# Optimization experiments

Measured on AMD Instinct MI355X. Metric: run time of the kernel, lower is better.

## Reference

```python
import jax, jax.numpy as jnp
import numpy as np
from jax.ops import segment_sum, segment_max

N, E, H, C = 20000, 320000, 4, 128
G, NF, EF, GF = 1024, 9, 4, 50
EPS = 1e-5
NEG_SLOPE = 0.2


def setup_inputs() -> dict:
    key = jax.random.key(0)
    ks = jax.random.split(key, 16)
    inp = {
        'x': jax.random.normal(ks[0], (N, NF), jnp.float32),
        'edge_attr': jax.random.normal(ks[1], (E, EF), jnp.float32),
        'global_feat': jax.random.normal(ks[2], (G, GF), jnp.float32),
        'Wl1': jax.random.normal(ks[3], (NF, H * C), jnp.float32) * 0.1,
        'Wr1': jax.random.normal(ks[4], (NF, H * C), jnp.float32) * 0.1,
        'We1': jax.random.normal(ks[5], (EF, H * C), jnp.float32) * 0.1,
        'att1': jax.random.normal(ks[6], (H, C), jnp.float32) * 0.1,
        'b1': jax.random.normal(ks[7], (H * C,), jnp.float32) * 0.01,
        'gamma1': jnp.ones((H * C,), jnp.float32),
        'beta1': jnp.zeros((H * C,), jnp.float32),
        'mean1': jnp.zeros((H * C,), jnp.float32),
        'var1': jnp.ones((H * C,), jnp.float32),
        'Wl2': jax.random.normal(ks[8], (H * C, H * C), jnp.float32) * 0.05,
        'Wr2': jax.random.normal(ks[9], (H * C, H * C), jnp.float32) * 0.05,
        'We2': jax.random.normal(ks[10], (EF, H * C), jnp.float32) * 0.1,
        'att2': jax.random.normal(ks[11], (H, C), jnp.float32) * 0.1,
        'b2': jax.random.normal(ks[12], (H * C,), jnp.float32) * 0.01,
        'gamma2': jnp.ones((H * C,), jnp.float32),
        'beta2': jnp.zeros((H * C,), jnp.float32),
        'mean2': jnp.zeros((H * C,), jnp.float32),
        'var2': jnp.ones((H * C,), jnp.float32),
        'fc1_w': jax.random.normal(ks[13], (H * C + GF, C), jnp.float32) * 0.05,
        'fc1_b': jnp.zeros((C,), jnp.float32),
        'fc2_w': jax.random.normal(ks[14], (C, 1), jnp.float32) * 0.1,
        'fc2_b': jnp.zeros((1,), jnp.float32),
        'edge_index': jax.random.randint(ks[15], (2, E), 0, N, jnp.int32),
        'batch': jnp.sort(jax.random.randint(jax.random.fold_in(key, 99), (N,), 0, G, jnp.int32)),
    }
    return inp


def gatv2_layer(x, src, dst, ea, Wl, Wr, We, att, bias):
    # PyG GATv2Conv: add self-loops with fill_value='mean' edge_attr
    n = x.shape[0]
    loop = jnp.arange(n, dtype=src.dtype)
    deg = segment_sum(jnp.ones((src.shape[0],), x.dtype), dst, num_segments=n)
    ea_mean = segment_sum(ea, dst, num_segments=n) / jnp.clip(deg, 1.0)[:, None]
    s = jnp.concatenate([src, loop])
    d = jnp.concatenate([dst, loop])
    eat = jnp.concatenate([ea, ea_mean], axis=0)
    xl = (x @ Wl).reshape(n, H, C)  # source transform
    xr = (x @ Wr).reshape(n, H, C)  # target transform
    ee = (eat @ We).reshape(-1, H, C)
    e = jax.nn.leaky_relu(xl[s] + xr[d] + ee, NEG_SLOPE)  # [E+N, H, C]
    logits = jnp.einsum('ehc,hc->eh', e, att)  # [E+N, H]
    m = segment_max(logits, d, num_segments=n)  # stable segment softmax
    ex = jnp.exp(logits - m[d])
    alpha = ex / segment_sum(ex, d, num_segments=n)[d]
    out = segment_sum(alpha[..., None] * xl[s], d, num_segments=n)  # [N, H, C]
    return out.reshape(n, H * C) + bias


def batch_norm(x, g, b, mu, var):
    return (x - mu) * jax.lax.rsqrt(var + EPS) * g + b


def reference(x, edge_attr, global_feat, Wl1, Wr1, We1, att1, b1, gamma1, beta1, mean1, var1,
              Wl2, Wr2, We2, att2, b2, gamma2, beta2, mean2, var2,
              fc1_w, fc1_b, fc2_w, fc2_b, edge_index, batch):
    src, dst = edge_index[0], edge_index[1]
    h = jax.nn.relu(batch_norm(gatv2_layer(x, src, dst, edge_attr, Wl1, Wr1, We1, att1, b1),
                               gamma1, beta1, mean1, var1))
    h = jax.nn.relu(batch_norm(gatv2_layer(h, src, dst, edge_attr, Wl2, Wr2, We2, att2, b2),
                               gamma2, beta2, mean2, var2))
    cnt = segment_sum(jnp.ones((h.shape[0],), h.dtype), batch, num_segments=G)
    pooled = segment_sum(h, batch, num_segments=G) / jnp.clip(cnt, 1.0)[:, None]  # [G, H*C]
    z = jnp.concatenate([pooled, global_feat], axis=1)
    z = jax.nn.relu(z @ fc1_w + fc1_b)
    return (z @ fc2_w + fc2_b).squeeze()
```

## Files before the change

### kernel.cpp

```cpp
#include <hip/hip_runtime.h>
#include <hip/hip_bf16.h>

#define Nn 20000
#define Ee 320000
#define Hh 4
#define Cc 128
#define HC 512
#define Gg 1024
#define NFt 9
#define EFt 4
#define GFt 50
#define EPSf 1e-5f
#define SLOPE 0.2f

typedef __attribute__((ext_vector_type(8))) short bf16x8;
typedef __attribute__((ext_vector_type(4))) float f32x4;
typedef __attribute__((ext_vector_type(2))) float f32x2;
typedef __attribute__((ext_vector_type(4))) unsigned ui32x4;

typedef const __attribute__((address_space(1))) unsigned char* gp1_t;
typedef __attribute__((address_space(3))) unsigned char* lp3_t;
__device__ __forceinline__ void gload16(const void* g, void* l) {
    __builtin_amdgcn_global_load_lds((gp1_t)g, (lp3_t)l, 16, 0, 0);
}

__device__ __forceinline__ float bf2f(short s) {
    return __uint_as_float(((unsigned)(unsigned short)s) << 16);
}

__device__ __forceinline__ f32x2 pkfma(f32x2 a, f32x2 b, f32x2 c) {
    f32x2 d;
    asm("v_pk_fma_f32 %0, %1, %2, %3" : "=v"(d) : "v"(a), "v"(b), "v"(c));
    return d;
}
__device__ __forceinline__ f32x2 pkadd(f32x2 a, f32x2 b) {
    f32x2 d;
    asm("v_pk_add_f32 %0, %1, %2" : "=v"(d) : "v"(a), "v"(b));
    return d;
}
__device__ __forceinline__ f32x2 pkmul(f32x2 a, f32x2 b) {
    f32x2 d;
    asm("v_pk_mul_f32 %0, %1, %2" : "=v"(d) : "v"(a), "v"(b));
    return d;
}
__device__ __forceinline__ int bperm(int byteaddr, int v) {
    return __builtin_amdgcn_ds_bpermute(byteaddr, v);
}
__device__ __forceinline__ float bpermf(int byteaddr, float v) {
    return __int_as_float(__builtin_amdgcn_ds_bpermute(byteaddr, __float_as_int(v)));
}

__global__ __launch_bounds__(256) void k_setup(
    const int* __restrict__ dst, int* __restrict__ deg, int* __restrict__ rank,
    const int* __restrict__ batch, int* __restrict__ gofs,
    const float* __restrict__ Wl2, const float* __restrict__ Wr2,
    __hip_bfloat16* __restrict__ Wt,
    const float* __restrict__ x, const float* __restrict__ Wl1,
    const float* __restrict__ Wr1, __hip_bfloat16* __restrict__ xl,
    __hip_bfloat16* __restrict__ xr) {
    __shared__ float tile[64][65];
    int b = blockIdx.x, t = threadIdx.x;
    if (b < 1250) {
        int e = b * 256 + t;
        if (e < Ee) rank[e] = atomicAdd(&deg[dst[e]], 1);
    } else if (b < 1329) {
        int i = (b - 1250) * 256 + t;
        if (i >= Nn) return;
        int bb = batch[i];
        if (i == 0) {
            for (int g = 0; g <= bb; ++g) gofs[g] = 0;
        } else {
            int bp = batch[i - 1];
            for (int g = bp + 1; g <= bb; ++g) gofs[g] = i;
        }
        if (i == Nn - 1) {
            for (int g = bb + 1; g <= Gg; ++g) gofs[g] = Nn;
        }
    } else if (b < 1457) {
        int tid = b - 1329;
        int tc = (tid >> 3) * 64;
        int tk = (tid & 7) * 64;
        int lc = t & 63, lr = t >> 6;
        const float* W = (tc < 512) ? Wl2 : Wr2;
        int cb = tc & 511;
#pragma unroll
        for (int i = 0; i < 16; ++i) {
            int r = lr * 16 + i;
            tile[r][lc] = W[(size_t)(tk + r) * 512 + cb + lc];
        }
        __syncthreads();
#pragma unroll
        for (int i = 0; i < 16; ++i) {
            int c = lr * 16 + i;
            Wt[(size_t)(tc + c) * 512 + tk + lc] = __float2bfloat16(tile[lc][c]);
        }
    } else {
        int l = t & 63, w = t >> 6;
        int ch0 = l * 8;
        int wid = (b - 1457) * 4 + w;
        int n0 = wid * 2, n1 = n0 + 1;
        float xa[NFt], xb[NFt];
#pragma unroll
        for (int f = 0; f < NFt; ++f) {
            xa[f] = x[n0 * NFt + f];
            xb[f] = x[n1 * NFt + f];
        }
        float a0[8] = {}, r0[8] = {}, a1[8] = {}, r1[8] = {};
#pragma unroll
        for (int f = 0; f < NFt; ++f) {
            f32x4 wl0 = *(const f32x4*)&Wl1[f * HC + ch0];
            f32x4 wl1 = *(const f32x4*)&Wl1[f * HC + ch0 + 4];
            f32x4 wr0 = *(const f32x4*)&Wr1[f * HC + ch0];
            f32x4 wr1 = *(const f32x4*)&Wr1[f * HC + ch0 + 4];
#pragma unroll
            for (int k = 0; k < 4; ++k) {
                a0[k] = fmaf(xa[f], wl0[k], a0[k]);
                a0[k + 4] = fmaf(xa[f], wl1[k], a0[k + 4]);
                r0[k] = fmaf(xa[f], wr0[k], r0[k]);
                r0[k + 4] = fmaf(xa[f], wr1[k], r0[k + 4]);
                a1[k] = fmaf(xb[f], wl0[k], a1[k]);
                a1[k + 4] = fmaf(xb[f], wl1[k], a1[k + 4]);
                r1[k] = fmaf(xb[f], wr0[k], r1[k]);
                r1[k + 4] = fmaf(xb[f], wr1[k], r1[k + 4]);
            }
        }
        auto cvt8 = [](const float* v) {
            bf16x8 o;
#pragma unroll
            for (int k = 0; k < 8; ++k) {
                union { float f; unsigned u; } cv;
                cv.f = v[k];
                unsigned r = (cv.u + 0x7fff + ((cv.u >> 16) & 1)) >> 16;
                o[k] = (short)r;
            }
            return o;
        };
        *(bf16x8*)(xl + (size_t)n0 * HC + ch0) = cvt8(a0);
        *(bf16x8*)(xr + (size_t)n0 * HC + ch0) = cvt8(r0);
        *(bf16x8*)(xl + (size_t)n1 * HC + ch0) = cvt8(a1);
        *(bf16x8*)(xr + (size_t)n1 * HC + ch0) = cvt8(r1);
    }
}

__global__ void k_scan(const int* __restrict__ deg, int* __restrict__ rowptr) {
    __shared__ int sums[1024];
    int t = threadIdx.x;
    const int n = Nn;
    int chunk = (n + 1023) / 1024;
    int start = t * chunk;
    int lim = min(start + chunk, n);
    int s = 0;
    for (int i = start; i < lim; ++i) s += deg[i];
    sums[t] = s;
    __syncthreads();
    for (int off = 1; off < 1024; off <<= 1) {
        int v = (t >= off) ? sums[t - off] : 0;
        __syncthreads();
        sums[t] += v;
        __syncthreads();
    }
    int run = (t == 0) ? 0 : sums[t - 1];
    for (int i = start; i < lim; ++i) { rowptr[i] = run; run += deg[i]; }
    if (t == 1023) rowptr[n] = sums[1023];
}

__global__ void k_scatter(const int* __restrict__ src, const int* __restrict__ dst,
                          const float* __restrict__ ea, const int* __restrict__ rowptr,
                          const int* __restrict__ rank, int* __restrict__ csr_src,
                          float4* __restrict__ ea_s) {
    int e = blockIdx.x * 256 + threadIdx.x;
    if (e >= Ee) return;
    int pos = rowptr[dst[e]] + rank[e];
    csr_src[pos] = src[e];
    ea_s[pos] = ((const float4*)ea)[e];
}

__global__ __launch_bounds__(256) void k_gemm_mfma(const short* __restrict__ Abf,
                                                   const short* __restrict__ Bt,
                                                   __hip_bfloat16* __restrict__ xl,
                                                   __hip_bfloat16* __restrict__ xr, int M) {
    __shared__ short As[128 * 32];
    __shared__ short Bs[128 * 32];
    int tid = threadIdx.x;
    int l = tid & 63;
    int wid = tid >> 6;
    int bm0 = blockIdx.x * 128;
    int bn0 = blockIdx.y * 128;
    int wr = (wid >> 1) * 64;
    int wc = (wid & 1) * 64;
    f32x4 acc[4][4] = {};

    int srow = l >> 2;
    int skoff = ((l & 3) ^ ((l >> 3) & 3)) * 8;
    int rk = (((l >> 4) ^ (l >> 1)) & 3) * 8;

    for (int k0 = 0; k0 < 512; k0 += 32) {
        {
            int c = wid;
            long row = min(bm0 + c * 16 + srow, M - 1);
            gload16(Abf + row * 512 + k0 + skoff, &As[c * 512]);
            int col = bn0 + c * 16 + srow;
            gload16(Bt + (size_t)col * 512 + k0 + skoff, &Bs[c * 512]);
            c = wid + 4;
            row = min(bm0 + c * 16 + srow, M - 1);
            gload16(Abf + row * 512 + k0 + skoff, &As[c * 512]);
            col = bn0 + c * 16 + srow;
            gload16(Bt + (size_t)col * 512 + k0 + skoff, &Bs[c * 512]);
        }
        asm volatile("s_waitcnt vmcnt(0)" ::: "memory");
        __syncthreads();
        bf16x8 af[4], bfr[4];
#pragma unroll
        for (int m = 0; m < 4; ++m)
            af[m] = *(const bf16x8*)&As[(wr + m * 16 + (l & 15)) * 32 + rk];
#pragma unroll
        for (int n = 0; n < 4; ++n)
            bfr[n] = *(const bf16x8*)&Bs[(wc + n * 16 + (l & 15)) * 32 + rk];
#pragma unroll
        for (int m = 0; m < 4; ++m)
#pragma unroll
            for (int n = 0; n < 4; ++n)
                acc[m][n] = __builtin_amdgcn_mfma_f32_16x16x32_bf16(af[m], bfr[n],
                                                                    acc[m][n], 0, 0, 0);
        __syncthreads();
    }
    __hip_bfloat16* dst = (bn0 < 512) ? xl : xr;
    int cb = bn0 & 511;
#pragma unroll
    for (int m = 0; m < 4; ++m) {
#pragma unroll
        for (int n = 0; n < 4; ++n) {
            int col = cb + wc + n * 16 + (l & 15);
#pragma unroll
            for (int r = 0; r < 4; ++r) {
                int row = bm0 + wr + m * 16 + (l >> 4) * 4 + r;
                if (row < M) dst[(size_t)row * 512 + col] = __float2bfloat16(acc[m][n][r]);
            }
        }
    }
}

__global__ __launch_bounds__(256) void k_fused_attn(
    const __hip_bfloat16* __restrict__ xl, const __hip_bfloat16* __restrict__ xr,
    const float* __restrict__ We, const float* __restrict__ att,
    const int* __restrict__ rowptr, const int* __restrict__ csr_src,
    const float4* __restrict__ ea_s, const float* __restrict__ bias,
    const float* __restrict__ gamma, const float* __restrict__ beta,
    const float* __restrict__ mean, const float* __restrict__ var,
    __hip_bfloat16* __restrict__ hout) {
    int n = blockIdx.x * 4 + (threadIdx.x >> 6);
    if (n >= Nn) return;
    int l = threadIdx.x & 63;
    int ch0 = l * 8;
    const unsigned char* xlb = (const unsigned char*)xl;
    int choff = ch0 * 2;

    f32x2 wee2[4][4], ar2[4], rr2[4];
#pragma unroll
    for (int f = 0; f < 4; ++f) {
        f32x4 w0 = *(const f32x4*)&We[f * HC + ch0];
        f32x4 w1 = *(const f32x4*)&We[f * HC + ch0 + 4];
        wee2[f][0] = (f32x2){w0.x, w0.y};
        wee2[f][1] = (f32x2){w0.z, w0.w};
        wee2[f][2] = (f32x2){w1.x, w1.y};
        wee2[f][3] = (f32x2){w1.z, w1.w};
    }
    {
        f32x4 a0 = *(const f32x4*)&att[ch0];
        f32x4 a1 = *(const f32x4*)&att[ch0 + 4];
        ar2[0] = (f32x2){a0.x, a0.y};
        ar2[1] = (f32x2){a0.z, a0.w};
        ar2[2] = (f32x2){a1.x, a1.y};
        ar2[3] = (f32x2){a1.z, a1.w};
    }
    {
        ui32x4 ru = *(const ui32x4*)(xr + (size_t)n * HC + ch0);
#pragma unroll
        for (int j = 0; j < 4; ++j) {
            unsigned u = ru[j];
            rr2[j] = (f32x2){__uint_as_float(u << 16), __uint_as_float(u & 0xffff0000u)};
        }
    }

    int start = __builtin_amdgcn_readfirstlane(rowptr[n]);
    int nedge = __builtin_amdgcn_readfirstlane(rowptr[n + 1]) - start;

    float m = -1e30f, den = 0.f;
    f32x2 acc2[4] = {};
    float esl0 = 0.f, esl1 = 0.f, esl2 = 0.f, esl3 = 0.f;

    struct Chunk {
        float e[4][4];
        bf16x8 x[4];
    };

    for (int mb = 0; mb < nedge; mb += 64) {
        int cnt = min(64, nedge - mb);
        int msrc = 0;
        float4 mea = make_float4(0.f, 0.f, 0.f, 0.f);
        if (l < cnt) {
            msrc = csr_src[start + mb + l];
            mea = ea_s[start + mb + l];
        }
        esl0 += mea.x; esl1 += mea.y; esl2 += mea.z; esl3 += mea.w;

        auto fetch = [&](Chunk& C, int fb) {
#pragma unroll
            for (int j = 0; j < 4; ++j) {
                int ba = min(fb + j, cnt - 1) * 4;
                int sj = bperm(ba, msrc);
                C.e[j][0] = bpermf(ba, mea.x);
                C.e[j][1] = bpermf(ba, mea.y);
                C.e[j][2] = bpermf(ba, mea.z);
                C.e[j][3] = bpermf(ba, mea.w);
                unsigned voff = ((unsigned)sj << 10) + choff;
                C.x[j] = *(const bf16x8*)(xlb + voff);
            }
        };

        auto compute = [&](const Chunk& C, int base) {
            float p[4];
#pragma unroll
            for (int i = 0; i < 4; ++i) {
                ui32x4 xu = *(const ui32x4*)&C.x[i];
                f32x2 e0p = (f32x2){C.e[i][0], C.e[i][0]};
                f32x2 e1p = (f32x2){C.e[i][1], C.e[i][1]};
                f32x2 e2p = (f32x2){C.e[i][2], C.e[i][2]};
                f32x2 e3p = (f32x2){C.e[i][3], C.e[i][3]};
                f32x2 plin = (f32x2){0.f, 0.f}, pabs = (f32x2){0.f, 0.f};
#pragma unroll
                for (int j = 0; j < 4; ++j) {
                    unsigned u = xu[j];
                    f32x2 xv = (f32x2){__uint_as_float(u << 16),
                                       __uint_as_float(u & 0xffff0000u)};
                    f32x2 z = pkadd(xv, rr2[j]);
                    z = pkfma(e0p, wee2[0][j], z);
                    z = pkfma(e1p, wee2[1][j], z);
                    z = pkfma(e2p, wee2[2][j], z);
                    z = pkfma(e3p, wee2[3][j], z);
                    f32x2 za = (f32x2){fabsf(z.x), fabsf(z.y)};
                    plin = pkfma(ar2[j], z, plin);
                    pabs = pkfma(ar2[j], za, pabs);
                }
                p[i] = 0.6f * (plin.x + plin.y) + 0.4f * (pabs.x + pabs.y);
            }
#pragma unroll
            for (int off = 8; off; off >>= 1) {
                p[0] += __shfl_xor(p[0], off);
                p[1] += __shfl_xor(p[1], off);
                p[2] += __shfl_xor(p[2], off);
                p[3] += __shfl_xor(p[3], off);
            }
#pragma unroll
            for (int i = 1; i < 4; ++i)
                if (base + i >= cnt) p[i] = -1e30f;

            float pmax = fmaxf(fmaxf(p[0], p[1]), fmaxf(p[2], p[3]));
            float ex[4];
            float mloc = m;
            if (!__all(pmax <= mloc + 8.f)) {
                float mn = fmaxf(mloc, pmax);
                float sc = __expf(mloc - mn);
                den *= sc;
                f32x2 scs = (f32x2){sc, sc};
#pragma unroll
                for (int j = 0; j < 4; ++j) acc2[j] = pkmul(acc2[j], scs);
                m = mn;
                mloc = mn;
            }
            ex[0] = __expf(p[0] - mloc); ex[1] = __expf(p[1] - mloc);
            ex[2] = __expf(p[2] - mloc); ex[3] = __expf(p[3] - mloc);
            den += ex[0] + ex[1] + ex[2] + ex[3];
#pragma unroll
            for (int i = 0; i < 4; ++i) {
                f32x2 esp = (f32x2){ex[i], ex[i]};
                ui32x4 xu = *(const ui32x4*)&C.x[i];
#pragma unroll
                for (int j = 0; j < 4; ++j) {
                    unsigned u = xu[j];
                    f32x2 xv = (f32x2){__uint_as_float(u << 16),
                                       __uint_as_float(u & 0xffff0000u)};
                    acc2[j] = pkfma(esp, xv, acc2[j]);
                }
            }
        };

        Chunk A, B;
        fetch(A, 0);
        int base = 0;
        for (;;) {
            fetch(B, base + 4);
            compute(A, base);
            base += 4;
            if (base >= cnt) break;
            fetch(A, base + 4);
            compute(B, base);
            base += 4;
            if (base >= cnt) break;
        }
    }

    {
#pragma unroll
        for (int off = 32; off; off >>= 1) {
            esl0 += __shfl_xor(esl0, off);
            esl1 += __shfl_xor(esl1, off);
            esl2 += __shfl_xor(esl2, off);
            esl3 += __shfl_xor(esl3, off);
        }
        float dv = 1.f / (float)max(nedge, 1);
        f32x2 e0p = (f32x2){esl0 * dv, esl0 * dv};
        f32x2 e1p = (f32x2){esl1 * dv, esl1 * dv};
        f32x2 e2p = (f32x2){esl2 * dv, esl2 * dv};
        f32x2 e3p = (f32x2){esl3 * dv, esl3 * dv};
        ui32x4 xu = *(const ui32x4*)(xl + (size_t)n * HC + ch0);
        f32x2 plin = (f32x2){0.f, 0.f}, pabs = (f32x2){0.f, 0.f};
        f32x2 xv2[4];
#pragma unroll
        for (int j = 0; j < 4; ++j) {
            unsigned u = xu[j];
            xv2[j] = (f32x2){__uint_as_float(u << 16), __uint_as_float(u & 0xffff0000u)};
            f32x2 z = pkadd(xv2[j], rr2[j]);
            z = pkfma(e0p, wee2[0][j], z);
            z = pkfma(e1p, wee2[1][j], z);
            z = pkfma(e2p, wee2[2][j], z);
            z = pkfma(e3p, wee2[3][j], z);
            f32x2 za = (f32x2){fabsf(z.x), fabsf(z.y)};
            plin = pkfma(ar2[j], z, plin);
            pabs = pkfma(ar2[j], za, pabs);
        }
        float pi = 0.6f * (plin.x + plin.y) + 0.4f * (pabs.x + pabs.y);
#pragma unroll
        for (int off = 8; off; off >>= 1) pi += __shfl_xor(pi, off);
        float mn = fmaxf(m, pi);
        float sc = __expf(m - mn);
        float ex = __expf(pi - mn);
        den = den * sc + ex;
        f32x2 scs = (f32x2){sc, sc};
        f32x2 exs = (f32x2){ex, ex};
#pragma unroll
        for (int j = 0; j < 4; ++j) acc2[j] = pkfma(exs, xv2[j], pkmul(acc2[j], scs));
    }

    float iden = 1.f / den;
    f32x4 bi0 = *(const f32x4*)&bias[ch0], bi1 = *(const f32x4*)&bias[ch0 + 4];
    f32x4 ga0 = *(const f32x4*)&gamma[ch0], ga1 = *(const f32x4*)&gamma[ch0 + 4];
    f32x4 be0 = *(const f32x4*)&beta[ch0], be1 = *(const f32x4*)&beta[ch0 + 4];
    f32x4 me0 = *(const f32x4*)&mean[ch0], me1 = *(const f32x4*)&mean[ch0 + 4];
    f32x4 va0 = *(const f32x4*)&var[ch0], va1 = *(const f32x4*)&var[ch0 + 4];
    float aflat[8] = {acc2[0].x, acc2[0].y, acc2[1].x, acc2[1].y,
                      acc2[2].x, acc2[2].y, acc2[3].x, acc2[3].y};
    bf16x8 ob;
#pragma unroll
    for (int k = 0; k < 8; ++k) {
        float bik = (k < 4) ? bi0[k] : bi1[k - 4];
        float gak = (k < 4) ? ga0[k] : ga1[k - 4];
        float bek = (k < 4) ? be0[k] : be1[k - 4];
        float mek = (k < 4) ? me0[k] : me1[k - 4];
        float vak = (k < 4) ? va0[k] : va1[k - 4];
        float Sk = gak * rsqrtf(vak + EPSf);
        float Ok = (bik - mek) * Sk + bek;
        float v = fmaxf(fmaf(aflat[k] * iden, Sk, Ok), 0.f);
        union { float f; unsigned u; } cv;
        cv.f = v;
        unsigned r = (cv.u + 0x7fff + ((cv.u >> 16) & 1)) >> 16;
        ob[k] = (short)r;
    }
    *(bf16x8*)(hout + (size_t)n * HC + ch0) = ob;
}

__global__ __launch_bounds__(256) void k_pool_mlp(
    const __hip_bfloat16* __restrict__ h, const int* __restrict__ gofs,
    const float* __restrict__ gfeat, const float* __restrict__ fc1w,
    const float* __restrict__ fc1b, const float* __restrict__ fc2w,
    const float* __restrict__ fc2b, float* __restrict__ out) {
    __shared__ float z[HC + GFt];
    __shared__ float red[256];
    int g = blockIdx.x, t = threadIdx.x;
    int s = gofs[g], e = gofs[g + 1];
    float a0 = 0.f, a1 = 0.f;
    for (int r = s; r < e; ++r) {
        ushort2 v = ((const ushort2*)(h + (size_t)r * HC))[t];
        a0 += bf2f((short)v.x);
        a1 += bf2f((short)v.y);
    }
    float ic = (e > s) ? 1.f / (float)(e - s) : 0.f;
    z[2 * t] = a0 * ic;
    z[2 * t + 1] = a1 * ic;
    if (t < GFt) z[HC + t] = gfeat[g * GFt + t];
    __syncthreads();
    int c = t & 127, half = t >> 7;
    float acc = (half == 0) ? fc1b[c] : 0.f;
    int j0 = half * 281, j1 = j0 + 281;
    for (int j = j0; j < j1; ++j) acc += z[j] * fc1w[j * 128 + c];
    red[t] = acc;
    __syncthreads();
    if (t < 128) {
        float a = red[t] + red[t + 128];
        red[t] = fmaxf(a, 0.f) * fc2w[t];
    }
    __syncthreads();
    for (int off = 64; off; off >>= 1) {
        if (t < off) red[t] += red[t + off];
        __syncthreads();
    }
    if (t == 0) out[g] = red[0] + fc2b[0];
}

extern "C" void kernel_launch(void* const* d_in, const int* in_sizes, int n_in,
                              void* d_out, int out_size, void* d_ws, size_t ws_size,
                              hipStream_t stream) {
    const float* x = (const float*)d_in[0];
    const float* ea = (const float*)d_in[1];
    const float* gfeat = (const float*)d_in[2];
    const float* Wl1 = (const float*)d_in[3];
    const float* Wr1 = (const float*)d_in[4];
    const float* We1 = (const float*)d_in[5];
    const float* att1 = (const float*)d_in[6];
    const float* b1 = (const float*)d_in[7];
    const float* gamma1 = (const float*)d_in[8];
    const float* beta1 = (const float*)d_in[9];
    const float* mean1 = (const float*)d_in[10];
    const float* var1 = (const float*)d_in[11];
    const float* Wl2 = (const float*)d_in[12];
    const float* Wr2 = (const float*)d_in[13];
    const float* We2 = (const float*)d_in[14];
    const float* att2 = (const float*)d_in[15];
    const float* b2 = (const float*)d_in[16];
    const float* gamma2 = (const float*)d_in[17];
    const float* beta2 = (const float*)d_in[18];
    const float* mean2 = (const float*)d_in[19];
    const float* var2 = (const float*)d_in[20];
    const float* fc1w = (const float*)d_in[21];
    const float* fc1b = (const float*)d_in[22];
    const float* fc2w = (const float*)d_in[23];
    const float* fc2b = (const float*)d_in[24];
    const int* eidx = (const int*)d_in[25];
    const int* batch = (const int*)d_in[26];
    float* out = (float*)d_out;

    const int* srcp = eidx;
    const int* dstp = eidx + Ee;

    char* p = (char*)d_ws;
    auto alloc = [&](size_t bytes) -> char* {
        char* r = p;
        p += (bytes + 255) & ~(size_t)255;
        return r;
    };
    __hip_bfloat16* xl = (__hip_bfloat16*)alloc((size_t)Nn * HC * 2);
    __hip_bfloat16* xr = (__hip_bfloat16*)alloc((size_t)Nn * HC * 2);
    __hip_bfloat16* h_bf = (__hip_bfloat16*)alloc((size_t)Nn * HC * 2);
    int* deg = (int*)alloc((size_t)Nn * 4);
    int* rank = (int*)alloc((size_t)Ee * 4);
    int* rowptr = (int*)alloc((size_t)(Nn + 1) * 4);
    int* csr_src = (int*)alloc((size_t)Ee * 4);
    float4* ea_s = (float4*)alloc((size_t)Ee * 16);
    int* gofs = (int*)alloc((size_t)(Gg + 1) * 4);
    __hip_bfloat16* Wt = (__hip_bfloat16*)alloc((size_t)1024 * 512 * 2);

    hipMemsetAsync(deg, 0, (size_t)Nn * 4, stream);

    k_setup<<<1457 + 2500, 256, 0, stream>>>(dstp, deg, rank, batch, gofs, Wl2, Wr2,
                                             Wt, x, Wl1, Wr1, xl, xr);
    k_scan<<<1, 1024, 0, stream>>>(deg, rowptr);
    k_scatter<<<(Ee + 255) / 256, 256, 0, stream>>>(srcp, dstp, ea, rowptr, rank,
                                                    csr_src, ea_s);

    k_fused_attn<<<(Nn + 3) / 4, 256, 0, stream>>>(xl, xr, We1, att1, rowptr, csr_src,
                                                   ea_s, b1, gamma1, beta1, mean1,
                                                   var1, h_bf);

    k_gemm_mfma<<<dim3((Nn + 127) / 128, 8), 256, 0, stream>>>(
        (const short*)h_bf, (const short*)Wt, xl, xr, Nn);
    k_fused_attn<<<(Nn + 3) / 4, 256, 0, stream>>>(xl, xr, We2, att2, rowptr, csr_src,
                                                   ea_s, b2, gamma2, beta2, mean2,
                                                   var2, h_bf);

    k_pool_mlp<<<Gg, 256, 0, stream>>>(h_bf, gofs, gfeat, fc1w, fc1b, fc2w, fc2b, out);
}
```

Before: 330.4 us.

## Replace bpermute edge-metadata broadcast with scalar readfirstlane loads and deeper prefetch

Each wave used to load 64 edges of metadata cooperatively and broadcast it with ds_bpermute. Now every lane loads the same edge indices and attributes, which are made wave-uniform with readfirstlane. A three-stage pipeline (issue metadata, commit to scalar, gather xl rows) runs across 4-edge chunks, and the self-loop mean is summed in-register without a cross-lane reduction. The aim is to remove LDS permute traffic and the per-64-edge block structure, at the cost of redundant per-lane metadata loads and more live registers. The grid size is also hardcoded to 5000, which equals the old expression.

```diff
diff --git a/kernel.cpp b/kernel.cpp
--- a/kernel.cpp
+++ b/kernel.cpp
@@ -27,6 +27,9 @@
 __device__ __forceinline__ float bf2f(short s) {
     return __uint_as_float(((unsigned)(unsigned short)s) << 16);
 }
+__device__ __forceinline__ float rfl(float v) {
+    return __uint_as_float(__builtin_amdgcn_readfirstlane(__float_as_uint(v)));
+}
 
 __device__ __forceinline__ f32x2 pkfma(f32x2 a, f32x2 b, f32x2 c) {
     f32x2 d;
@@ -42,12 +45,6 @@
     f32x2 d;
     asm("v_pk_mul_f32 %0, %1, %2" : "=v"(d) : "v"(a), "v"(b));
     return d;
-}
-__device__ __forceinline__ int bperm(int byteaddr, int v) {
-    return __builtin_amdgcn_ds_bpermute(byteaddr, v);
-}
-__device__ __forceinline__ float bpermf(int byteaddr, float v) {
-    return __int_as_float(__builtin_amdgcn_ds_bpermute(byteaddr, __float_as_int(v)));
 }
 
 __global__ __launch_bounds__(256) void k_setup(
@@ -252,8 +249,6 @@
     if (n >= Nn) return;
     int l = threadIdx.x & 63;
     int ch0 = l * 8;
-    const unsigned char* xlb = (const unsigned char*)xl;
-    int choff = ch0 * 2;
 
     f32x2 wee2[4][4], ar2[4], rr2[4];
 #pragma unroll
@@ -284,136 +279,162 @@
 
     int start = __builtin_amdgcn_readfirstlane(rowptr[n]);
     int nedge = __builtin_amdgcn_readfirstlane(rowptr[n + 1]) - start;
+    int last = start + nedge - 1;
 
     float m = -1e30f, den = 0.f;
     f32x2 acc2[4] = {};
-    float esl0 = 0.f, esl1 = 0.f, esl2 = 0.f, esl3 = 0.f;
-
-    struct Chunk {
+    float es0 = 0.f, es1 = 0.f, es2 = 0.f, es3 = 0.f;
+
+    struct MetaV {
+        int s[4];
+        float4 e[4];
+    };
+    struct MetaS {
+        int s[4];
+        float e[4][4];
+    };
+    struct Xc {
         float e[4][4];
         bf16x8 x[4];
     };
 
-    for (int mb = 0; mb < nedge; mb += 64) {
-        int cnt = min(64, nedge - mb);
-        int msrc = 0;
-        float4 mea = make_float4(0.f, 0.f, 0.f, 0.f);
-        if (l < cnt) {
-            msrc = csr_src[start + mb + l];
-            mea = ea_s[start + mb + l];
-        }
-        esl0 += mea.x; esl1 += mea.y; esl2 += mea.z; esl3 += mea.w;
-
-        auto fetch = [&](Chunk& C, int fb) {
+    auto issue_meta = [&](MetaV& mv, int b4) {
+#pragma unroll
+        for (int i = 0; i < 4; ++i) {
+            int idx = min(start + b4 + i, last);
+            mv.s[i] = csr_src[idx];
+            mv.e[i] = ea_s[idx];
+        }
+    };
+    auto commit_meta = [&](MetaS& ms, const MetaV& mv) {
+#pragma unroll
+        for (int i = 0; i < 4; ++i) {
+            ms.s[i] = __builtin_amdgcn_readfirstlane(mv.s[i]);
+            ms.e[i][0] = rfl(mv.e[i].x);
+            ms.e[i][1] = rfl(mv.e[i].y);
+            ms.e[i][2] = rfl(mv.e[i].z);
+            ms.e[i][3] = rfl(mv.e[i].w);
+        }
+    };
+    auto gather = [&](Xc& X, const MetaS& ms) {
+#pragma unroll
+        for (int i = 0; i < 4; ++i) {
+            X.x[i] = *(const bf16x8*)(xl + (size_t)ms.s[i] * HC + ch0);
+#pragma unroll
+            for (int j = 0; j < 4; ++j) X.e[i][j] = ms.e[i][j];
+        }
+    };
+    auto compute = [&](const Xc& C, int base) {
+#pragma unroll
+        for (int i = 0; i < 4; ++i) {
+            if (base + i < nedge) {
+                es0 += C.e[i][0]; es1 += C.e[i][1];
+                es2 += C.e[i][2]; es3 += C.e[i][3];
+            }
+        }
+        float p[4];
+#pragma unroll
+        for (int i = 0; i < 4; ++i) {
+            ui32x4 xu = *(const ui32x4*)&C.x[i];
+            f32x2 e0p = (f32x2){C.e[i][0], C.e[i][0]};
+            f32x2 e1p = (f32x2){C.e[i][1], C.e[i][1]};
+            f32x2 e2p = (f32x2){C.e[i][2], C.e[i][2]};
+            f32x2 e3p = (f32x2){C.e[i][3], C.e[i][3]};
+            f32x2 plin = (f32x2){0.f, 0.f}, pabs = (f32x2){0.f, 0.f};
 #pragma unroll
             for (int j = 0; j < 4; ++j) {
-                int ba = min(fb + j, cnt - 1) * 4;
-                int sj = bperm(ba, msrc);
-                C.e[j][0] = bpermf(ba, mea.x);
-                C.e[j][1] = bpermf(ba, mea.y);
-                C.e[j][2] = bpermf(ba, mea.z);
-                C.e[j][3] = bpermf(ba, mea.w);
-                unsigned voff = ((unsigned)sj << 10) + choff;
-                C.x[j] = *(const bf16x8*)(xlb + voff);
+                unsigned u = xu[j];
+                f32x2 xv = (f32x2){__uint_as_float(u << 16),
+                                   __uint_as_float(u & 0xffff0000u)};
+                f32x2 z = pkadd(xv, rr2[j]);
+                z = pkfma(e0p, wee2[0][j], z);
+                z = pkfma(e1p, wee2[1][j], z);
+                z = pkfma(e2p, wee2[2][j], z);
+                z = pkfma(e3p, wee2[3][j], z);
+                f32x2 za = (f32x2){fabsf(z.x), fabsf(z.y)};
+                plin = pkfma(ar2[j], z, plin);
+                pabs = pkfma(ar2[j], za, pabs);
             }
-        };
-
-        auto compute = [&](const Chunk& C, int base) {
-            float p[4];
-#pragma unroll
-            for (int i = 0; i < 4; ++i) {
-                ui32x4 xu = *(const ui32x4*)&C.x[i];
-                f32x2 e0p = (f32x2){C.e[i][0], C.e[i][0]};
-                f32x2 e1p = (f32x2){C.e[i][1], C.e[i][1]};
-                f32x2 e2p = (f32x2){C.e[i][2], C.e[i][2]};
-                f32x2 e3p = (f32x2){C.e[i][3], C.e[i][3]};
-                f32x2 plin = (f32x2){0.f, 0.f}, pabs = (f32x2){0.f, 0.f};
-#pragma unroll
-                for (int j = 0; j < 4; ++j) {
-                    unsigned u = xu[j];
-                    f32x2 xv = (f32x2){__uint_as_float(u << 16),
-                                       __uint_as_float(u & 0xffff0000u)};
-                    f32x2 z = pkadd(xv, rr2[j]);
-                    z = pkfma(e0p, wee2[0][j], z);
-                    z = pkfma(e1p, wee2[1][j], z);
-                    z = pkfma(e2p, wee2[2][j], z);
-                    z = pkfma(e3p, wee2[3][j], z);
-                    f32x2 za = (f32x2){fabsf(z.x), fabsf(z.y)};
-                    plin = pkfma(ar2[j], z, plin);
-                    pabs = pkfma(ar2[j], za, pabs);
-                }
-                p[i] = 0.6f * (plin.x + plin.y) + 0.4f * (pabs.x + pabs.y);
+            p[i] = 0.6f * (plin.x + plin.y) + 0.4f * (pabs.x + pabs.y);
+        }
+#pragma unroll
+        for (int off = 8; off; off >>= 1) {
+            p[0] += __shfl_xor(p[0], off);
+            p[1] += __shfl_xor(p[1], off);
+            p[2] += __shfl_xor(p[2], off);
+            p[3] += __shfl_xor(p[3], off);
+        }
+#pragma unroll
+        for (int i = 1; i < 4; ++i)
+            if (base + i >= nedge) p[i] = -1e30f;
+
+        float pmax = fmaxf(fmaxf(p[0], p[1]), fmaxf(p[2], p[3]));
+        float ex[4];
+        float mloc = m;
+        if (!__all(pmax <= mloc + 8.f)) {
+            float mn = fmaxf(mloc, pmax);
+            float sc = __expf(mloc - mn);
+            den *= sc;
+            f32x2 scs = (f32x2){sc, sc};
+#pragma unroll
+            for (int j = 0; j < 4; ++j) acc2[j] = pkmul(acc2[j], scs);
+            m = mn;
+            mloc = mn;
+        }
+        ex[0] = __expf(p[0] - mloc); ex[1] = __expf(p[1] - mloc);
+        ex[2] = __expf(p[2] - mloc); ex[3] = __expf(p[3] - mloc);
+        den += ex[0] + ex[1] + ex[2] + ex[3];
+#pragma unroll
+        for (int i = 0; i < 4; ++i) {
+            f32x2 esp = (f32x2){ex[i], ex[i]};
+            ui32x4 xu = *(const ui32x4*)&C.x[i];
+#pragma unroll
+            for (int j = 0; j < 4; ++j) {
+                unsigned u = xu[j];
+                f32x2 xv = (f32x2){__uint_as_float(u << 16),
+                                   __uint_as_float(u & 0xffff0000u)};
+                acc2[j] = pkfma(esp, xv, acc2[j]);
             }
-#pragma unroll
-            for (int off = 8; off; off >>= 1) {
-                p[0] += __shfl_xor(p[0], off);
-                p[1] += __shfl_xor(p[1], off);
-                p[2] += __shfl_xor(p[2], off);
-                p[3] += __shfl_xor(p[3], off);
-            }
-#pragma unroll
-            for (int i = 1; i < 4; ++i)
-                if (base + i >= cnt) p[i] = -1e30f;
-
-            float pmax = fmaxf(fmaxf(p[0], p[1]), fmaxf(p[2], p[3]));
-            float ex[4];
-            float mloc = m;
-            if (!__all(pmax <= mloc + 8.f)) {
-                float mn = fmaxf(mloc, pmax);
-                float sc = __expf(mloc - mn);
-                den *= sc;
-                f32x2 scs = (f32x2){sc, sc};
-#pragma unroll
-                for (int j = 0; j < 4; ++j) acc2[j] = pkmul(acc2[j], scs);
-                m = mn;
-                mloc = mn;
-            }
-            ex[0] = __expf(p[0] - mloc); ex[1] = __expf(p[1] - mloc);
-            ex[2] = __expf(p[2] - mloc); ex[3] = __expf(p[3] - mloc);
-            den += ex[0] + ex[1] + ex[2] + ex[3];
-#pragma unroll
-            for (int i = 0; i < 4; ++i) {
-                f32x2 esp = (f32x2){ex[i], ex[i]};
-                ui32x4 xu = *(const ui32x4*)&C.x[i];
-#pragma unroll
-                for (int j = 0; j < 4; ++j) {
-                    unsigned u = xu[j];
-                    f32x2 xv = (f32x2){__uint_as_float(u << 16),
-                                       __uint_as_float(u & 0xffff0000u)};
-                    acc2[j] = pkfma(esp, xv, acc2[j]);
-                }
-            }
-        };
-
-        Chunk A, B;
-        fetch(A, 0);
+        }
+    };
+
+    if (nedge > 0) {
+        MetaV mvi;
+        MetaS msN;
+        Xc XA, XB;
+        issue_meta(mvi, 0);
+        {
+            MetaS ms0;
+            commit_meta(ms0, mvi);
+            issue_meta(mvi, 4);
+            gather(XA, ms0);
+        }
+        commit_meta(msN, mvi);
+        issue_meta(mvi, 8);
+
         int base = 0;
         for (;;) {
-            fetch(B, base + 4);
-            compute(A, base);
+            gather(XB, msN);
+            commit_meta(msN, mvi);
+            issue_meta(mvi, base + 12);
+            compute(XA, base);
             base += 4;
-            if (base >= cnt) break;
-            fetch(A, base + 4);
-            compute(B, base);
+            if (base >= nedge) break;
+            gather(XA, msN);
+            commit_meta(msN, mvi);
+            issue_meta(mvi, base + 12);
+            compute(XB, base);
             base += 4;
-            if (base >= cnt) break;
+            if (base >= nedge) break;
         }
     }
 
     {
-#pragma unroll
-        for (int off = 32; off; off >>= 1) {
-            esl0 += __shfl_xor(esl0, off);
-            esl1 += __shfl_xor(esl1, off);
-            esl2 += __shfl_xor(esl2, off);
-            esl3 += __shfl_xor(esl3, off);
-        }
-        float dv = 1.f / (float)max(nedge, 1);
-        f32x2 e0p = (f32x2){esl0 * dv, esl0 * dv};
-        f32x2 e1p = (f32x2){esl1 * dv, esl1 * dv};
-        f32x2 e2p = (f32x2){esl2 * dv, esl2 * dv};
-        f32x2 e3p = (f32x2){esl3 * dv, esl3 * dv};
+        float dv = (float)max(nedge, 1);
+        float e0 = es0 / dv, e1 = es1 / dv, e2 = es2 / dv, e3 = es3 / dv;
         ui32x4 xu = *(const ui32x4*)(xl + (size_t)n * HC + ch0);
+        f32x2 e0p = (f32x2){e0, e0}, e1p = (f32x2){e1, e1};
+        f32x2 e2p = (f32x2){e2, e2}, e3p = (f32x2){e3, e3};
         f32x2 plin = (f32x2){0.f, 0.f}, pabs = (f32x2){0.f, 0.f};
         f32x2 xv2[4];
 #pragma unroll
@@ -567,15 +588,15 @@
     k_scatter<<<(Ee + 255) / 256, 256, 0, stream>>>(srcp, dstp, ea, rowptr, rank,
                                                     csr_src, ea_s);
 
-    k_fused_attn<<<(Nn + 3) / 4, 256, 0, stream>>>(xl, xr, We1, att1, rowptr, csr_src,
-                                                   ea_s, b1, gamma1, beta1, mean1,
-                                                   var1, h_bf);
+    k_fused_attn<<<5000, 256, 0, stream>>>(xl, xr, We1, att1, rowptr, csr_src,
+                                           ea_s, b1, gamma1, beta1, mean1, var1,
+                                           h_bf);
 
     k_gemm_mfma<<<dim3((Nn + 127) / 128, 8), 256, 0, stream>>>(
         (const short*)h_bf, (const short*)Wt, xl, xr, Nn);
-    k_fused_attn<<<(Nn + 3) / 4, 256, 0, stream>>>(xl, xr, We2, att2, rowptr, csr_src,
-                                                   ea_s, b2, gamma2, beta2, mean2,
-                                                   var2, h_bf);
+    k_fused_attn<<<5000, 256, 0, stream>>>(xl, xr, We2, att2, rowptr, csr_src,
+                                           ea_s, b2, gamma2, beta2, mean2, var2,
+                                           h_bf);
 
     k_pool_mlp<<<Gg, 256, 0, stream>>>(h_bf, gofs, gfeat, fc1w, fc1b, fc2w, fc2b, out);
 }
```

After: 316.8 us. 1.04x faster.
